# Kernel tuning notes

Measured on AMD Instinct MI355X. Metric: run time of the kernel, lower is better.

The kernel has to match this reference:

```python
import jax, jax.numpy as jnp
import numpy as np

N, L, E, NB, H = 128, 200, 128, 2, 2
ITEM = 50000
TEMP = 0.2
HD = E // H


def _ln(x, g, b, eps=1e-8):
    m = x.mean(-1, keepdims=True)
    v = ((x - m) ** 2).mean(-1, keepdims=True)
    return (x - m) / jnp.sqrt(v + eps) * g + b


def setup_inputs() -> dict:
    key = jax.random.key(0)
    ks = jax.random.split(key, 20)
    rng = np.random.default_rng(0)
    log_seqs = rng.integers(1, ITEM + 1, size=(N, L))
    lens = rng.integers(20, L + 1, size=(N,))
    log_seqs[np.arange(L)[None, :] < (L - lens[:, None])] = 0  # left padding, id 0
    pos_seqs = rng.integers(1, ITEM + 1, size=(N, L))
    neg_seqs = rng.integers(1, ITEM + 1, size=(N, L))
    item_emb = jax.random.normal(ks[0], (ITEM + 1, E), jnp.float32) * 0.02
    item_emb = item_emb.at[0].set(0.0)  # padding_idx=0
    s = 1.0 / np.sqrt(E)
    return {
        "item_emb": item_emb,
        "pos_emb": jax.random.normal(ks[1], (L + 1, E), jnp.float32) * 0.02,
        "W_asp": jax.random.normal(ks[2], (16, E, E), jnp.float32) * s,
        "w_weight": jax.random.normal(ks[3], (2 * E,), jnp.float32) * (1.0 / np.sqrt(2 * E)),
        "w_bias": jnp.zeros((), jnp.float32),
        "attn_ln_g": jnp.ones((NB, E), jnp.float32),
        "attn_ln_b": jnp.zeros((NB, E), jnp.float32),
        "in_proj_w": jax.random.normal(ks[4], (NB, 3 * E, E), jnp.float32) * s,
        "in_proj_b": jnp.zeros((NB, 3 * E), jnp.float32),
        "out_proj_w": jax.random.normal(ks[5], (NB, E, E), jnp.float32) * s,
        "out_proj_b": jnp.zeros((NB, E), jnp.float32),
        "fwd_ln_g": jnp.ones((NB, E), jnp.float32),
        "fwd_ln_b": jnp.zeros((NB, E), jnp.float32),
        "conv1_w": jax.random.normal(ks[6], (NB, E, E), jnp.float32) * s,
        "conv1_b": jnp.zeros((NB, E), jnp.float32),
        "conv2_w": jax.random.normal(ks[7], (NB, E, E), jnp.float32) * s,
        "conv2_b": jnp.zeros((NB, E), jnp.float32),
        "last_ln_g": jnp.ones((E,), jnp.float32),
        "last_ln_b": jnp.zeros((E,), jnp.float32),
        "user_ids": jnp.asarray(rng.integers(0, 100000, size=(N,)), jnp.int32),
        "log_seqs": jnp.asarray(log_seqs, jnp.int32),
        "pos_seqs": jnp.asarray(pos_seqs, jnp.int32),
        "neg_seqs": jnp.asarray(neg_seqs, jnp.int32),
        "epoch": 1,
    }


def reference(item_emb, pos_emb, W_asp, w_weight, w_bias, attn_ln_g, attn_ln_b,
              in_proj_w, in_proj_b, out_proj_w, out_proj_b, fwd_ln_g, fwd_ln_b,
              conv1_w, conv1_b, conv2_w, conv2_b, last_ln_g, last_ln_b,
              user_ids, log_seqs, pos_seqs, neg_seqs, epoch):
    tmask = (log_seqs == 0)                               # (N,L) True=pad
    validL = (~tmask).astype(item_emb.dtype)              # (N,L)
    seqs0 = item_emb[log_seqs] * validL[..., None]
    pos_embs = item_emb[pos_seqs] * validL[..., None]
    neg_embs = item_emb[neg_seqs] * validL[..., None]

    validE = jnp.concatenate([validL, validL[:, -1:]], 1)  # (N,L+1)
    kv_save = jnp.concatenate([seqs0, pos_embs[:, -1:, :]], 1)  # (N,L+1,E)

    def aspects(x, valid, residual):
        a = jnp.einsum('nli,aoi->nlao', x, W_asp)          # 16 expert GEMMs batched
        if residual:
            a = a + x[:, :, None, :]
            a = a / (jnp.linalg.norm(a, axis=-1, keepdims=True) + 1e-8)
        return a * valid[:, :, None, None]

    kv4 = aspects(kv_save, validE, True)                   # (N,L+1,16,E)
    temp = aspects(kv_save, validE, False)
    nvalid = validE.sum()
    cent_loss = jnp.linalg.norm(kv_save * validE[..., None] - temp.mean(2), axis=-1).sum() / nvalid

    norm_x = kv4 / (jnp.linalg.norm(kv4, axis=-1, keepdims=True) + 1e-8)
    pos_s = (norm_x * norm_x).sum(-1)                      # (N,L+1,16)
    ttl = jnp.einsum('nlae,nlbe->nlab', norm_x, norm_x)    # pairwise cosine sims
    mi = -(pos_s / TEMP - jnp.log(jnp.exp(ttl / TEMP).sum(-1)))
    ind_loss = (mi * validE[:, :, None]).sum() / nvalid

    s = kv4.sum(2)                                         # (N,L+1,E)
    q = jnp.cumsum(s, 1) - s                               # exclusive cumsum
    cnt = jnp.cumsum(validE, 1) - validE
    q = q / (16.0 * cnt + 1e-8)[..., None] * validE[..., None]

    w_q, w_a = w_weight[:E], w_weight[E:]

    def gate(qv, a4):                                      # learned softmax gating
        logits = (qv @ w_q)[:, :, None] + a4 @ w_a + w_bias
        w = jax.nn.softmax(logits, axis=2)
        return (a4 * w[..., None]).sum(2)

    re_all = gate(q, kv4)                                  # (N,L+1,E)
    re_emb = re_all[:, :L] + kv4[:, :L].mean(2)

    neg_kv4 = aspects(neg_embs, validL, True)
    q2 = q[:, 1:, :] * validL[..., None]
    neg_t = gate(q2, neg_kv4) + neg_kv4.mean(2)
    pos_t = re_all[:, 1:, :] * validL[..., None] + (kv4[:, 1:] * validL[..., None, None]).mean(2)

    seqs = re_emb * (E ** 0.5) + pos_emb[jnp.arange(L)][None]
    seqs = seqs * validL[..., None]
    causal = jnp.where(jnp.tril(jnp.ones((L, L), bool)), 0.0, -1e9)
    scale = HD ** -0.5
    for i in range(NB):
        Qn = _ln(seqs, attn_ln_g[i], attn_ln_b[i])
        qp = Qn @ in_proj_w[i][:E].T + in_proj_b[i][:E]
        kp = seqs @ in_proj_w[i][E:2 * E].T + in_proj_b[i][E:2 * E]
        vp = seqs @ in_proj_w[i][2 * E:].T + in_proj_b[i][2 * E:]
        sp = lambda x: x.reshape(N, L, H, HD).transpose(0, 2, 1, 3)
        att = jax.nn.softmax(jnp.einsum('nhqd,nhkd->nhqk', sp(qp), sp(kp)) * scale + causal, axis=-1)
        o = jnp.einsum('nhqk,nhkd->nhqd', att, sp(vp)).transpose(0, 2, 1, 3).reshape(N, L, E)
        seqs = Qn + (o @ out_proj_w[i].T + out_proj_b[i])
        seqs = _ln(seqs, fwd_ln_g[i], fwd_ln_b[i])
        h = jax.nn.relu(seqs @ conv1_w[i].T + conv1_b[i])
        seqs = (h @ conv2_w[i].T + conv2_b[i]) + seqs
        seqs = seqs * validL[..., None]
    log_feats = _ln(seqs, last_ln_g, last_ln_b)
    pos_logits = (log_feats * pos_t).sum(-1)
    neg_logits = (log_feats * neg_t).sum(-1)
    return (pos_logits, neg_logits, ind_loss, cent_loss)
```

## Files before the change

### kernel.cpp

```cpp
#include <hip/hip_runtime.h>
#include <hip/hip_bf16.h>
#include <cstddef>

typedef __attribute__((ext_vector_type(8))) short bf16x8;
typedef __attribute__((ext_vector_type(4))) float f32x4;
typedef unsigned short ushort_t;

__device__ __forceinline__ short f2bf(float f) {
    __hip_bfloat16 h = __float2bfloat16(f);
    return __builtin_bit_cast(short, h);
}
__device__ __forceinline__ float bf2f(short s) {
    unsigned u = ((unsigned)(unsigned short)s) << 16;
    return __builtin_bit_cast(float, u);
}
__device__ __forceinline__ unsigned pk2(float a, float b) {
    return (unsigned)(unsigned short)f2bf(a) | ((unsigned)(unsigned short)f2bf(b) << 16);
}

__global__ void cvt_all(const float* __restrict__ s0, const float* __restrict__ s1,
                        const float* __restrict__ s2, const float* __restrict__ s3,
                        const float* __restrict__ s4, ushort_t* __restrict__ dst) {
    const int i = blockIdx.x * 256 + threadIdx.x;
    const int mat = i >> 14;
    const int wm = i & 16383;
    const int blk = wm >> 9;
    const int t = blk >> 2, f = blk & 3;
    const int lane = (wm >> 3) & 63;
    const int j = wm & 7;
    const int g4 = lane >> 4, nn = lane & 15;
    const int srcoff = (t * 16 + nn) * 128 + f * 32 + g4 * 8 + j;
    const float* src; int mbase;
    if (mat < 16)      { src = s0; mbase = mat; }
    else if (mat < 22) { src = s1; mbase = mat - 16; }
    else if (mat < 24) { src = s2; mbase = mat - 22; }
    else if (mat < 26) { src = s3; mbase = mat - 24; }
    else               { src = s4; mbase = mat - 26; }
    dst[i] = (ushort_t)f2bf(src[(size_t)mbase * 16384 + srcoff]);
}

__global__ __launch_bounds__(512, 1) void aspects2_kernel(
        const float* __restrict__ item_emb,
        const int* __restrict__ log_seqs, const int* __restrict__ pos_seqs,
        const int* __restrict__ neg_seqs,
        const ushort_t* __restrict__ Wab,
        const float* __restrict__ w_weight,
        const float* __restrict__ pos_emb,
        float* __restrict__ Gout, float* __restrict__ seqs,
        float* __restrict__ validE, float* __restrict__ validL,
        float* __restrict__ pInd, float* __restrict__ pCent,
        int nLossBlocks) {
    __shared__ ushort_t rsb[32 * 2184];
    __shared__ ushort_t xsb[32 * 136];
    __shared__ ushort_t wal_b[128];
    __shared__ int sidx[32];
    __shared__ float s_red[512];
    __shared__ float s_lg[512];
    __shared__ float s_pos[512];
    __shared__ float vld[32];
    __shared__ float centw[32];
    __shared__ float miw[32];

    const int tid = threadIdx.x;
    const int row0 = blockIdx.x * 32;
    const bool losses = (int)blockIdx.x < nLossBlocks;
    const int lane = tid & 63, w = tid >> 6;
    const int g4 = lane >> 4, nn = lane & 15;

    if (tid < 32) {
        const int rg = row0 + tid;
        int si; float vl;
        if (rg < 25728) {
            const int nq = rg / 201, l = rg % 201;
            if (l < 200) { si = log_seqs[nq * 200 + l]; vl = (si != 0) ? 1.f : 0.f; }
            else { vl = (log_seqs[nq * 200 + 199] != 0) ? 1.f : 0.f; si = pos_seqs[nq * 200 + 199]; }
            validE[rg] = vl;
        } else {
            const int rr = rg - 25728;
            vl = (log_seqs[rr] != 0) ? 1.f : 0.f;
            si = neg_seqs[rr];
            validL[rr] = vl;
        }
        sidx[tid] = si;
        vld[tid] = vl;
    }
    if (tid < 128) wal_b[tid] = (ushort_t)f2bf(w_weight[128 + tid]);
    __syncthreads();

    {
        const int r = tid >> 4, c8 = (tid & 15) * 8;
        const float vl = vld[r];
        const float* px = &item_emb[(size_t)sidx[r] * 128 + c8];
        const float4 a = *(const float4*)px;
        const float4 b = *(const float4*)(px + 4);
        *(int2*)&xsb[r * 136 + c8] = make_int2(
            (int)pk2(a.x * vl, a.y * vl), (int)pk2(a.z * vl, a.w * vl));
        *(int2*)&xsb[r * 136 + c8 + 4] = make_int2(
            (int)pk2(b.x * vl, b.y * vl), (int)pk2(b.z * vl, b.w * vl));
    }
    __syncthreads();

    bf16x8 xf0[4], xf1[4], waf[4];
#pragma unroll
    for (int f = 0; f < 4; ++f) {
        xf0[f] = *(const bf16x8*)&xsb[nn * 136 + f * 32 + g4 * 8];
        xf1[f] = *(const bf16x8*)&xsb[(nn + 16) * 136 + f * 32 + g4 * 8];
        waf[f] = *(const bf16x8*)&wal_b[f * 32 + g4 * 8];
    }

    for (int al = 0; al < 2; ++al) {
        const int a = w * 2 + al;
        const ushort_t* wbase = Wab + (size_t)a * 16384 + lane * 8;
#pragma unroll
        for (int t = 0; t < 8; ++t) {
            f32x4 d0 = {0.f, 0.f, 0.f, 0.f}, d1 = d0;
#pragma unroll
            for (int f = 0; f < 4; ++f) {
                bf16x8 wf = *(const bf16x8*)&wbase[(t * 4 + f) * 512];
                d0 = __builtin_amdgcn_mfma_f32_16x16x32_bf16(wf, xf0[f], d0, 0, 0, 0);
                d1 = __builtin_amdgcn_mfma_f32_16x16x32_bf16(wf, xf1[f], d1, 0, 0, 0);
            }
            const int o0 = t * 16 + g4 * 4;
            const int xs0 = o0 & 4;
            {
                const bf16x8 xb = *(const bf16x8*)&xsb[nn * 136 + (o0 & ~7)];
                *(int2*)&rsb[nn * 2184 + a * 136 + o0] = make_int2(
                    (int)pk2(d0[0] + bf2f(xb[xs0]),     d0[1] + bf2f(xb[xs0 + 1])),
                    (int)pk2(d0[2] + bf2f(xb[xs0 + 2]), d0[3] + bf2f(xb[xs0 + 3])));
            }
            {
                const bf16x8 xb = *(const bf16x8*)&xsb[(nn + 16) * 136 + (o0 & ~7)];
                *(int2*)&rsb[(nn + 16) * 2184 + a * 136 + o0] = make_int2(
                    (int)pk2(d1[0] + bf2f(xb[xs0]),     d1[1] + bf2f(xb[xs0 + 1])),
                    (int)pk2(d1[2] + bf2f(xb[xs0 + 2]), d1[3] + bf2f(xb[xs0 + 3])));
            }
        }
    }
    __syncthreads();

    f32x4 gram0 = {0.f,0.f,0.f,0.f}, gram1 = gram0, gram2 = gram0, gram3 = gram0;
#pragma unroll
    for (int rl = 0; rl < 4; ++rl) {
        const int row = w * 4 + rl;
        f32x4 dgr = {0.f, 0.f, 0.f, 0.f}, dlp = dgr;
#pragma unroll
        for (int f = 0; f < 4; ++f) {
            bf16x8 fr = *(const bf16x8*)&rsb[row * 2184 + nn * 136 + f * 32 + g4 * 8];
            dgr = __builtin_amdgcn_mfma_f32_16x16x32_bf16(fr, fr, dgr, 0, 0, 0);
            dlp = __builtin_amdgcn_mfma_f32_16x16x32_bf16(fr, waf[f], dlp, 0, 0, 0);
        }
        if (rl == 0) gram0 = dgr; else if (rl == 1) gram1 = dgr;
        else if (rl == 2) gram2 = dgr; else gram3 = dgr;
        if (g4 == (nn >> 2)) s_red[row * 16 + nn] = dgr[nn & 3];
        if (nn == 0) {
#pragma unroll
            for (int r = 0; r < 4; ++r) s_lg[row * 16 + g4 * 4 + r] = dlp[r];
        }
    }
    __syncthreads();

    {
        const float nrm = sqrtf(s_red[tid]);
        const float inv1 = 1.f / (nrm + 1e-8f);
        const float n2 = nrm * inv1;
        const float sg = inv1 / (n2 + 1e-8f);
        const float ts = n2 / (n2 + 1e-8f);
        const float logit = s_lg[tid] * inv1;
        float mx = logit;
#pragma unroll
        for (int m = 1; m < 16; m <<= 1) mx = fmaxf(mx, __shfl_xor(mx, m, 16));
        const float e = __expf(logit - mx);
        float ssum = e;
#pragma unroll
        for (int m = 1; m < 16; m <<= 1) ssum += __shfl_xor(ssum, m, 16);
        s_red[tid] = sg;
        s_pos[tid] = ts * ts * 5.f;
        s_lg[tid] = (e / ssum + 0.0625f) * inv1;
    }
    __syncthreads();

    {
        const int row = tid >> 4, ol = tid & 15, o8 = ol * 8;
        float g[8] = {0.f, 0.f, 0.f, 0.f, 0.f, 0.f, 0.f, 0.f};
        float sr[8] = {0.f, 0.f, 0.f, 0.f, 0.f, 0.f, 0.f, 0.f};
#pragma unroll
        for (int a = 0; a < 16; ++a) {
            const bf16x8 vb = *(const bf16x8*)&rsb[row * 2184 + a * 136 + o8];
            const float gw = s_lg[row * 16 + a];
#pragma unroll
            for (int j = 0; j < 8; ++j) {
                const float v = bf2f(vb[j]);
                g[j] += v * gw;
                if (losses) sr[j] += v;
            }
        }
        float* go = &Gout[(size_t)(row0 + row) * 128 + o8];
        *(float4*)go       = make_float4(g[0], g[1], g[2], g[3]);
        *(float4*)(go + 4) = make_float4(g[4], g[5], g[6], g[7]);
        if (losses) {
            const int rg = row0 + row;
            const int nq = rg / 201, l = rg % 201;
            if (l < 200) {
                const float4 p0 = *(const float4*)&pos_emb[l * 128 + o8];
                const float4 p1 = *(const float4*)&pos_emb[l * 128 + o8 + 4];
                const float vv = vld[row];
                float* so = &seqs[(size_t)(nq * 200 + l) * 128 + o8];
                const float SQ = 11.313708498984761f;
                *(float4*)so = make_float4((g[0] * SQ + p0.x) * vv, (g[1] * SQ + p0.y) * vv,
                                           (g[2] * SQ + p0.z) * vv, (g[3] * SQ + p0.w) * vv);
                *(float4*)(so + 4) = make_float4((g[4] * SQ + p1.x) * vv, (g[5] * SQ + p1.y) * vv,
                                                 (g[6] * SQ + p1.z) * vv, (g[7] * SQ + p1.w) * vv);
            }
            const bf16x8 xb = *(const bf16x8*)&xsb[row * 136 + o8];
            float c = 0.f;
#pragma unroll
            for (int j = 0; j < 8; ++j) {
                const float dd = 2.f * bf2f(xb[j]) - sr[j] * 0.0625f;
                c += dd * dd;
            }
            c += __shfl_xor(c, 1, 64);
            c += __shfl_xor(c, 2, 64);
            c += __shfl_xor(c, 4, 64);
            c += __shfl_xor(c, 8, 64);
            if (ol == 0) centw[row] = sqrtf(c) * vld[row];
        }
    }

    if (losses) {
#pragma unroll
        for (int rl = 0; rl < 4; ++rl) {
            const int row = w * 4 + rl;
            const f32x4 dd = (rl == 0) ? gram0 : (rl == 1) ? gram1 : (rl == 2) ? gram2 : gram3;
            const float sgb = s_red[row * 16 + nn];
            float mis = 0.f;
#pragma unroll
            for (int r = 0; r < 4; ++r) {
                const int a = g4 * 4 + r;
                const float sga = s_red[row * 16 + a];
                float eb = __expf(5.f * dd[r] * sga * sgb);
#pragma unroll
                for (int m = 1; m < 16; m <<= 1) eb += __shfl_xor(eb, m, 16);
                mis += -(s_pos[row * 16 + a] - logf(eb));
            }
            mis += __shfl_xor(mis, 16, 64);
            mis += __shfl_xor(mis, 32, 64);
            if (lane == 0) miw[row] = mis * vld[row];
        }
        __syncthreads();
        if (tid == 0) {
            float si = 0.f, sc = 0.f;
#pragma unroll
            for (int r = 0; r < 32; ++r) { si += miw[r]; sc += centw[r]; }
            pInd[blockIdx.x] = si;
            pCent[blockIdx.x] = sc;
        }
    }
}

__global__ __launch_bounds__(256) void qkv_kernel(const float* __restrict__ X,
                                                  const ushort_t* __restrict__ W3,
                                                  const float* __restrict__ b3,
                                                  const float* __restrict__ lng,
                                                  const float* __restrict__ lnb,
                                                  float* __restrict__ Xn,
                                                  ushort_t* __restrict__ qo,
                                                  ushort_t* __restrict__ ko,
                                                  ushort_t* __restrict__ vo) {
    const int tid = threadIdx.x, lane = tid & 63, w = tid >> 6;
    const int q = lane >> 4, nn = lane & 15;
    const int m0 = blockIdx.x * 64 + w * 16;
    float xv[4][8];
    float s = 0.f, sq = 0.f;
    const float* xr = &X[(size_t)(m0 + nn) * 128];
#pragma unroll
    for (int f = 0; f < 4; ++f) {
        const float4 a = *(const float4*)&xr[f * 32 + q * 8];
        const float4 b = *(const float4*)&xr[f * 32 + q * 8 + 4];
        xv[f][0] = a.x; xv[f][1] = a.y; xv[f][2] = a.z; xv[f][3] = a.w;
        xv[f][4] = b.x; xv[f][5] = b.y; xv[f][6] = b.z; xv[f][7] = b.w;
        s += (a.x + a.y) + (a.z + a.w) + (b.x + b.y) + (b.z + b.w);
        sq += (a.x * a.x + a.y * a.y) + (a.z * a.z + a.w * a.w)
            + (b.x * b.x + b.y * b.y) + (b.z * b.z + b.w * b.w);
    }
    bf16x8 afr[4];
#pragma unroll
    for (int f = 0; f < 4; ++f) {
        bf16x8 v;
#pragma unroll
        for (int j = 0; j < 8; ++j) v[j] = f2bf(xv[f][j]);
        afr[f] = v;
    }
    s += __shfl_xor(s, 16, 64);  s += __shfl_xor(s, 32, 64);
    sq += __shfl_xor(sq, 16, 64); sq += __shfl_xor(sq, 32, 64);
    const float mean = s * 0.0078125f;
    const float var = fmaxf(sq * 0.0078125f - mean * mean, 0.f);
    const float inv = rsqrtf(var + 1e-8f);
    bf16x8 afq[4];
#pragma unroll
    for (int f = 0; f < 4; ++f) {
        const int c0 = f * 32 + q * 8;
        const float4 ga = *(const float4*)&lng[c0];
        const float4 gb = *(const float4*)&lng[c0 + 4];
        const float4 ba = *(const float4*)&lnb[c0];
        const float4 bb = *(const float4*)&lnb[c0 + 4];
        float y[8];
        y[0] = (xv[f][0] - mean) * inv * ga.x + ba.x;
        y[1] = (xv[f][1] - mean) * inv * ga.y + ba.y;
        y[2] = (xv[f][2] - mean) * inv * ga.z + ba.z;
        y[3] = (xv[f][3] - mean) * inv * ga.w + ba.w;
        y[4] = (xv[f][4] - mean) * inv * gb.x + bb.x;
        y[5] = (xv[f][5] - mean) * inv * gb.y + bb.y;
        y[6] = (xv[f][6] - mean) * inv * gb.z + bb.z;
        y[7] = (xv[f][7] - mean) * inv * gb.w + bb.w;
        float* xo = &Xn[(size_t)(m0 + nn) * 128 + c0];
        *(float4*)xo       = make_float4(y[0], y[1], y[2], y[3]);
        *(float4*)(xo + 4) = make_float4(y[4], y[5], y[6], y[7]);
        bf16x8 v;
#pragma unroll
        for (int j = 0; j < 8; ++j) v[j] = f2bf(y[j]);
        afq[f] = v;
    }
    ushort_t* const outs[3] = {qo, ko, vo};
#pragma unroll
    for (int mi = 0; mi < 3; ++mi) {
        const ushort_t* wbase = W3 + (size_t)mi * 16384 + lane * 8;
        f32x4 acc[8];
#pragma unroll
        for (int t = 0; t < 8; ++t) acc[t] = (f32x4){0.f, 0.f, 0.f, 0.f};
#pragma unroll
        for (int t = 0; t < 8; ++t) {
#pragma unroll
            for (int f = 0; f < 4; ++f) {
                bf16x8 b = *(const bf16x8*)&wbase[(t * 4 + f) * 512];
                acc[t] = __builtin_amdgcn_mfma_f32_16x16x32_bf16(
                    (mi == 0) ? afq[f] : afr[f], b, acc[t], 0, 0, 0);
            }
        }
        const float* bi = b3 + mi * 128;
        ushort_t* outp = outs[mi];
#pragma unroll
        for (int t = 0; t < 8; ++t) {
            const int n = t * 16 + nn;
            const float bv = bi[n];
#pragma unroll
            for (int r = 0; r < 4; ++r) {
                const int row = m0 + q * 4 + r;
                outp[(size_t)row * 128 + n] = (ushort_t)f2bf(acc[t][r] + bv);
            }
        }
    }
}

__global__ __launch_bounds__(256) void ffn_kernel(const ushort_t* __restrict__ attno,
                                                  const ushort_t* __restrict__ outWb,
                                                  const float* __restrict__ outB,
                                                  const float* __restrict__ resQn,
                                                  const float* __restrict__ lng,
                                                  const float* __restrict__ lnb,
                                                  const ushort_t* __restrict__ c1wb,
                                                  const float* __restrict__ c1b,
                                                  const ushort_t* __restrict__ c2wb,
                                                  const float* __restrict__ c2b,
                                                  const float* __restrict__ validL,
                                                  float* __restrict__ seqs) {
    __shared__ ushort_t hls[64 * 136];
    const int tid = threadIdx.x, lane = tid & 63, w = tid >> 6;
    const int q = lane >> 4, nn = lane & 15;
    const int m0 = blockIdx.x * 64 + w * 16;
    const int wrow = w * 16;

    bf16x8 af[4];
    {
        const ushort_t* xb = &attno[(size_t)(m0 + nn) * 128];
#pragma unroll
        for (int f = 0; f < 4; ++f) af[f] = *(const bf16x8*)&xb[f * 32 + q * 8];
    }
    f32x4 acc[8];
#pragma unroll
    for (int t = 0; t < 8; ++t) acc[t] = (f32x4){0.f, 0.f, 0.f, 0.f};
    {
        const ushort_t* wbase = outWb + lane * 8;
#pragma unroll
        for (int t = 0; t < 8; ++t)
#pragma unroll
            for (int f = 0; f < 4; ++f) {
                bf16x8 b = *(const bf16x8*)&wbase[(t * 4 + f) * 512];
                acc[t] = __builtin_amdgcn_mfma_f32_16x16x32_bf16(af[f], b, acc[t], 0, 0, 0);
            }
    }
    float y[8][4];
    float s[4] = {0.f, 0.f, 0.f, 0.f}, sq[4] = {0.f, 0.f, 0.f, 0.f};
#pragma unroll
    for (int t = 0; t < 8; ++t) {
        const int n = t * 16 + nn;
        const float bi = outB[n];
#pragma unroll
        for (int r = 0; r < 4; ++r) {
            const float v = acc[t][r] + bi + resQn[(size_t)(m0 + q * 4 + r) * 128 + n];
            y[t][r] = v;
            s[r] += v;
            sq[r] += v * v;
        }
    }
#pragma unroll
    for (int m = 1; m < 16; m <<= 1) {
#pragma unroll
        for (int r = 0; r < 4; ++r) {
            s[r] += __shfl_xor(s[r], m, 64);
            sq[r] += __shfl_xor(sq[r], m, 64);
        }
    }
#pragma unroll
    for (int r = 0; r < 4; ++r) {
        const float mean = s[r] * 0.0078125f;
        const float var = fmaxf(sq[r] * 0.0078125f - mean * mean, 0.f);
        const float inv = rsqrtf(var + 1e-8f);
        s[r] = mean; sq[r] = inv;
    }
#pragma unroll
    for (int t = 0; t < 8; ++t) {
        const int n = t * 16 + nn;
        const float g = lng[n], b = lnb[n];
#pragma unroll
        for (int r = 0; r < 4; ++r) {
            const float v = (y[t][r] - s[r]) * sq[r] * g + b;
            y[t][r] = v;
            hls[(wrow + q * 4 + r) * 136 + n] = (ushort_t)f2bf(v);
        }
    }
    __syncthreads();
    {
        const ushort_t* xb = &hls[(wrow + nn) * 136];
#pragma unroll
        for (int f = 0; f < 4; ++f) af[f] = *(const bf16x8*)&xb[f * 32 + q * 8];
    }
    f32x4 acc2[8];
#pragma unroll
    for (int t = 0; t < 8; ++t) acc2[t] = (f32x4){0.f, 0.f, 0.f, 0.f};
    {
        const ushort_t* wbase = c1wb + lane * 8;
#pragma unroll
        for (int t = 0; t < 8; ++t)
#pragma unroll
            for (int f = 0; f < 4; ++f) {
                bf16x8 b = *(const bf16x8*)&wbase[(t * 4 + f) * 512];
                acc2[t] = __builtin_amdgcn_mfma_f32_16x16x32_bf16(af[f], b, acc2[t], 0, 0, 0);
            }
    }
    __syncthreads();
#pragma unroll
    for (int t = 0; t < 8; ++t) {
        const int n = t * 16 + nn;
        const float bi = c1b[n];
#pragma unroll
        for (int r = 0; r < 4; ++r)
            hls[(wrow + q * 4 + r) * 136 + n] = (ushort_t)f2bf(fmaxf(acc2[t][r] + bi, 0.f));
    }
    __syncthreads();
    {
        const ushort_t* xb = &hls[(wrow + nn) * 136];
#pragma unroll
        for (int f = 0; f < 4; ++f) af[f] = *(const bf16x8*)&xb[f * 32 + q * 8];
    }
    f32x4 acc3[8];
#pragma unroll
    for (int t = 0; t < 8; ++t) acc3[t] = (f32x4){0.f, 0.f, 0.f, 0.f};
    {
        const ushort_t* wbase = c2wb + lane * 8;
#pragma unroll
        for (int t = 0; t < 8; ++t)
#pragma unroll
            for (int f = 0; f < 4; ++f) {
                bf16x8 b = *(const bf16x8*)&wbase[(t * 4 + f) * 512];
                acc3[t] = __builtin_amdgcn_mfma_f32_16x16x32_bf16(af[f], b, acc3[t], 0, 0, 0);
            }
    }
    float mk[4];
#pragma unroll
    for (int r = 0; r < 4; ++r) mk[r] = validL[m0 + q * 4 + r];
#pragma unroll
    for (int t = 0; t < 8; ++t) {
        const int n = t * 16 + nn;
        const float bi = c2b[n];
#pragma unroll
        for (int r = 0; r < 4; ++r) {
            const int row = m0 + q * 4 + r;
            seqs[(size_t)row * 128 + n] = (acc3[t][r] + bi + y[t][r]) * mk[r];
        }
    }
}

__global__ void reduce_kernel(const float* __restrict__ pInd, const float* __restrict__ pCent,
                              int nblk, const float* __restrict__ validE, int nve,
                              float* __restrict__ outp) {
    __shared__ float a1[256], a2[256], a3[256];
    const int tid = threadIdx.x;
    float si = 0.f, sc = 0.f, nv = 0.f;
    for (int t = tid; t < nblk; t += 256) { si += pInd[t]; sc += pCent[t]; }
    for (int t = tid; t < nve; t += 256) nv += validE[t];
    a1[tid] = si; a2[tid] = sc; a3[tid] = nv;
    __syncthreads();
    for (int s = 128; s > 0; s >>= 1) {
        if (tid < s) { a1[tid] += a1[tid + s]; a2[tid] += a2[tid + s]; a3[tid] += a3[tid + s]; }
        __syncthreads();
    }
    if (tid == 0) { outp[0] = a1[0] / a3[0]; outp[1] = a2[0] / a3[0]; }
}

__global__ __launch_bounds__(256) void attn_kernel(const ushort_t* __restrict__ qp,
                                                   const ushort_t* __restrict__ kp,
                                                   const ushort_t* __restrict__ vp,
                                                   ushort_t* __restrict__ outp) {
    __shared__ ushort_t KsU[2048];
    __shared__ ushort_t VtU[2560];
    __shared__ ushort_t Pb[2560];

    const int tid = threadIdx.x, lane = tid & 63, w = tid >> 6;
    const int b = blockIdx.x;
    const int nh = b >> 2, qt = b & 3;
    const int n = nh >> 1, h = nh & 1;
    const size_t base = (size_t)n * 200 * 128 + (size_t)h * 64;
    const int qw = qt * 64 + w * 16;
    const bool wactive = qw < 200;
    const int q15 = lane & 15, g4 = lane >> 4;
    const int qglob = qw + q15;

    bf16x8 qf[2];
    {
        const int qr = (qglob < 200) ? qglob : 199;
#pragma unroll
        for (int f = 0; f < 2; ++f)
            qf[f] = *(const bf16x8*)&qp[base + (size_t)qr * 128 + f * 32 + g4 * 8];
    }
    f32x4 Oacc[4];
#pragma unroll
    for (int nt = 0; nt < 4; ++nt) Oacc[nt] = (f32x4){0.f, 0.f, 0.f, 0.f};
    float mrun = -1e30f, lrun = 0.f;

    const int kmax = min(200, qt * 64 + 64);
    ushort_t* PbW = Pb + w * 640;

    for (int jt = 0; jt < kmax; jt += 32) {
        __syncthreads();
        {
            const int k = tid >> 3, e0 = (tid & 7) * 8;
            const int krow = jt + k;
            int4 a = make_int4(0, 0, 0, 0);
            if (krow < 200) a = *(const int4*)&kp[base + (size_t)krow * 128 + e0];
            *(int4*)&KsU[(k * 128 + ((e0 * 2) ^ ((k & 7) << 4))) >> 1] = a;
        }
        {
            const int k = tid & 31, e0 = (tid >> 5) * 8;
            const int vrow = jt + k;
            int4 a = make_int4(0, 0, 0, 0);
            if (vrow < 200) a = *(const int4*)&vp[base + (size_t)vrow * 128 + e0];
            VtU[(e0 + 0) * 40 + k] = (ushort_t)((unsigned)a.x & 0xFFFF);
            VtU[(e0 + 1) * 40 + k] = (ushort_t)((unsigned)a.x >> 16);
            VtU[(e0 + 2) * 40 + k] = (ushort_t)((unsigned)a.y & 0xFFFF);
            VtU[(e0 + 3) * 40 + k] = (ushort_t)((unsigned)a.y >> 16);
            VtU[(e0 + 4) * 40 + k] = (ushort_t)((unsigned)a.z & 0xFFFF);
            VtU[(e0 + 5) * 40 + k] = (ushort_t)((unsigned)a.z >> 16);
            VtU[(e0 + 6) * 40 + k] = (ushort_t)((unsigned)a.w & 0xFFFF);
            VtU[(e0 + 7) * 40 + k] = (ushort_t)((unsigned)a.w >> 16);
        }
        __syncthreads();
        if (!wactive) continue;

        f32x4 d0 = {0.f, 0.f, 0.f, 0.f}, d1 = d0;
#pragma unroll
        for (int f = 0; f < 2; ++f) {
            const int ebyte = g4 * 16 + f * 64;
            const int sw = ebyte ^ ((q15 & 7) << 4);
            bf16x8 a0 = *(const bf16x8*)&KsU[(q15 * 128 + sw) >> 1];
            bf16x8 a1 = *(const bf16x8*)&KsU[((q15 + 16) * 128 + sw) >> 1];
            d0 = __builtin_amdgcn_mfma_f32_16x16x32_bf16(a0, qf[f], d0, 0, 0, 0);
            d1 = __builtin_amdgcn_mfma_f32_16x16x32_bf16(a1, qf[f], d1, 0, 0, 0);
        }
        const int kb = jt + g4 * 4;
        float p[8];
        float tmax = -1e30f;
#pragma unroll
        for (int r = 0; r < 4; ++r) {
            const float s0 = (kb + r      <= qglob) ? d0[r] * 0.125f : -1e30f;
            const float s1 = (kb + r + 16 <= qglob) ? d1[r] * 0.125f : -1e30f;
            p[r] = s0; p[r + 4] = s1;
            tmax = fmaxf(tmax, fmaxf(s0, s1));
        }
        tmax = fmaxf(tmax, __shfl_xor(tmax, 16, 64));
        tmax = fmaxf(tmax, __shfl_xor(tmax, 32, 64));
        const float mnew = fmaxf(mrun, tmax);
        const float corr = __expf(mrun - mnew);
        mrun = mnew;
        float tsum = 0.f;
#pragma unroll
        for (int i = 0; i < 8; ++i) {
            float pe = __expf(p[i] - mnew);
            pe = bf2f(f2bf(pe));
            p[i] = pe;
            tsum += pe;
        }
        tsum += __shfl_xor(tsum, 16, 64);
        tsum += __shfl_xor(tsum, 32, 64);
        lrun = lrun * corr + tsum;
        const int kl = g4 * 4;
        *(unsigned*)&PbW[q15 * 40 + kl]          = pk2(p[0], p[1]);
        *(unsigned*)&PbW[q15 * 40 + kl + 2]      = pk2(p[2], p[3]);
        *(unsigned*)&PbW[q15 * 40 + 16 + kl]     = pk2(p[4], p[5]);
        *(unsigned*)&PbW[q15 * 40 + 16 + kl + 2] = pk2(p[6], p[7]);
        asm volatile("" ::: "memory");
        float corr_r[4];
#pragma unroll
        for (int r = 0; r < 4; ++r) corr_r[r] = __shfl(corr, g4 * 4 + r, 64);
#pragma unroll
        for (int nt = 0; nt < 4; ++nt) {
#pragma unroll
            for (int r = 0; r < 4; ++r) Oacc[nt][r] *= corr_r[r];
        }
        bf16x8 pa = *(const bf16x8*)&PbW[q15 * 40 + g4 * 8];
#pragma unroll
        for (int nt = 0; nt < 4; ++nt) {
            bf16x8 vb = *(const bf16x8*)&VtU[(nt * 16 + q15) * 40 + g4 * 8];
            Oacc[nt] = __builtin_amdgcn_mfma_f32_16x16x32_bf16(pa, vb, Oacc[nt], 0, 0, 0);
        }
    }
    if (wactive) {
        float linv[4];
#pragma unroll
        for (int r = 0; r < 4; ++r) linv[r] = 1.f / __shfl(lrun, g4 * 4 + r, 64);
#pragma unroll
        for (int r = 0; r < 4; ++r) {
            const int qg = qw + g4 * 4 + r;
            if (qg < 200) {
#pragma unroll
                for (int nt = 0; nt < 4; ++nt)
                    outp[base + (size_t)qg * 128 + nt * 16 + q15] =
                        (ushort_t)f2bf(Oacc[nt][r] * linv[r]);
            }
        }
    }
}

__global__ __launch_bounds__(256) void logits_kernel(const float* __restrict__ seqs,
                                                     const float* __restrict__ lastg,
                                                     const float* __restrict__ lastb,
                                                     const float* __restrict__ G,
                                                     const float* __restrict__ negt,
                                                     const float* __restrict__ validL,
                                                     float* __restrict__ outp) {
    const int row = blockIdx.x * 4 + (threadIdx.x >> 6);
    const int lane = threadIdx.x & 63;
    if (row >= 25600) return;
    const int n = row / 200, j = row % 200;
    const float2 x = *(const float2*)&seqs[(size_t)row * 128 + lane * 2];
    float s = x.x + x.y, sq = x.x * x.x + x.y * x.y;
#pragma unroll
    for (int m = 1; m < 64; m <<= 1) { s += __shfl_xor(s, m, 64); sq += __shfl_xor(sq, m, 64); }
    const float mean = s * 0.0078125f;
    const float var = fmaxf(sq * 0.0078125f - mean * mean, 0.f);
    const float inv = rsqrtf(var + 1e-8f);
    const float2 gg = *(const float2*)&lastg[lane * 2];
    const float2 bb = *(const float2*)&lastb[lane * 2];
    const float y0 = (x.x - mean) * inv * gg.x + bb.x;
    const float y1 = (x.y - mean) * inv * gg.y + bb.y;
    const float2 g2 = *(const float2*)&G[((size_t)n * 201 + j + 1) * 128 + lane * 2];
    const float2 t2 = *(const float2*)&negt[(size_t)row * 128 + lane * 2];
    float sp = y0 * g2.x + y1 * g2.y;
    float sn = y0 * t2.x + y1 * t2.y;
#pragma unroll
    for (int m = 1; m < 64; m <<= 1) { sp += __shfl_xor(sp, m, 64); sn += __shfl_xor(sn, m, 64); }
    if (lane == 0) { outp[row] = sp * validL[row]; outp[25600 + row] = sn; }
}

extern "C" void kernel_launch(void* const* d_in, const int* in_sizes, int n_in,
                              void* d_out, int out_size, void* d_ws, size_t ws_size,
                              hipStream_t stream) {
    (void)in_sizes; (void)n_in; (void)out_size; (void)ws_size;
    const float* item_emb = (const float*)d_in[0];
    const float* pos_emb  = (const float*)d_in[1];
    const float* W_asp    = (const float*)d_in[2];
    const float* w_weight = (const float*)d_in[3];
    const float* attn_g = (const float*)d_in[5];
    const float* attn_b = (const float*)d_in[6];
    const float* inW    = (const float*)d_in[7];
    const float* inB    = (const float*)d_in[8];
    const float* outW   = (const float*)d_in[9];
    const float* outB   = (const float*)d_in[10];
    const float* fwd_g  = (const float*)d_in[11];
    const float* fwd_b  = (const float*)d_in[12];
    const float* c1w    = (const float*)d_in[13];
    const float* c1b    = (const float*)d_in[14];
    const float* c2w    = (const float*)d_in[15];
    const float* c2b    = (const float*)d_in[16];
    const float* last_g = (const float*)d_in[17];
    const float* last_b = (const float*)d_in[18];
    const int* log_seqs = (const int*)d_in[20];
    const int* pos_seqs = (const int*)d_in[21];
    const int* neg_seqs = (const int*)d_in[22];

    float* ws = (float*)d_ws;
    const size_t S = (size_t)128 * 201 * 128;
    ushort_t* qp = (ushort_t*)ws;
    ushort_t* kp = qp + (size_t)25600 * 128;
    float* G     = ws + 2 * S;
    float* negt  = ws + 3 * S;
    float* seqs  = ws + 4 * S;
    float* Qn    = ws + 5 * S;
    ushort_t* vp    = (ushort_t*)(ws + 6 * S);
    ushort_t* attno = (ushort_t*)(ws + 7 * S);
    ushort_t* wb  = (ushort_t*)(ws + 8 * S);
    ushort_t* Wab  = wb;
    ushort_t* inWb = Wab + 262144;
    ushort_t* outWb = inWb + 98304;
    ushort_t* c1b_w = outWb + 32768;
    ushort_t* c2b_w = c1b_w + 32768;
    float* validE = ws + 8 * S + 229376;
    float* validL = validE + 128 * 201;
    float* pInd   = validL + 128 * 200;
    float* pCent  = pInd + 804;
    float* outF   = (float*)d_out;

    cvt_all<<<dim3(1792), dim3(256), 0, stream>>>(W_asp, inW, outW, c1w, c2w, wb);
    aspects2_kernel<<<dim3(1604), dim3(512), 0, stream>>>(
        item_emb, log_seqs, pos_seqs, neg_seqs, Wab, w_weight, pos_emb,
        G, seqs, validE, validL, pInd, pCent, 804);
    reduce_kernel<<<dim3(1), dim3(256), 0, stream>>>(
        pInd, pCent, 804, validE, 128 * 201, outF + 51200);

    for (int i = 0; i < 2; ++i) {
        qkv_kernel<<<dim3(400), dim3(256), 0, stream>>>(
            seqs, inWb + (size_t)i * 3 * 16384, inB + (size_t)i * 384,
            attn_g + i * 128, attn_b + i * 128, Qn, qp, kp, vp);
        attn_kernel<<<dim3(1024), dim3(256), 0, stream>>>(qp, kp, vp, attno);
        ffn_kernel<<<dim3(400), dim3(256), 0, stream>>>(
            attno, outWb + (size_t)i * 16384, outB + i * 128, Qn,
            fwd_g + i * 128, fwd_b + i * 128,
            c1b_w + (size_t)i * 16384, c1b + i * 128,
            c2b_w + (size_t)i * 16384, c2b + i * 128,
            validL, seqs);
    }
    logits_kernel<<<dim3(6400), dim3(256), 0, stream>>>(
        seqs, last_g, last_b, G, negt, validL, outF);
}
```

Baseline: 218.5 us.

## Fuse final layernorm and logits into last FFN, fold residual into aspect weights

The final layer norm and pos/neg logit dot products now run inside the last FFN kernel's epilogue, using 16-lane shuffles over the MFMA accumulators. This removes the separate logits kernel and the write and re-read of seqs for the last block. Separately, the aspect-projection residual (x + W x) is folded into the bf16 weight conversion by adding an identity to W_asp, so the per-element add from shared memory disappears from the aspects kernel. The fused epilogue reads G and negt with scattered per-lane loads, and adding 1.0 to the diagonal before bf16 rounding slightly changes numerics.

```diff
diff --git a/kernel.cpp b/kernel.cpp
--- a/kernel.cpp
+++ b/kernel.cpp
@@ -29,14 +29,18 @@
     const int lane = (wm >> 3) & 63;
     const int j = wm & 7;
     const int g4 = lane >> 4, nn = lane & 15;
-    const int srcoff = (t * 16 + nn) * 128 + f * 32 + g4 * 8 + j;
+    const int o = t * 16 + nn;
+    const int k = f * 32 + g4 * 8 + j;
+    const int srcoff = o * 128 + k;
     const float* src; int mbase;
     if (mat < 16)      { src = s0; mbase = mat; }
     else if (mat < 22) { src = s1; mbase = mat - 16; }
     else if (mat < 24) { src = s2; mbase = mat - 22; }
     else if (mat < 26) { src = s3; mbase = mat - 24; }
     else               { src = s4; mbase = mat - 26; }
-    dst[i] = (ushort_t)f2bf(src[(size_t)mbase * 16384 + srcoff]);
+    float v = src[(size_t)mbase * 16384 + srcoff];
+    if (mat < 16 && o == k) v += 1.f;
+    dst[i] = (ushort_t)f2bf(v);
 }
 
 __global__ __launch_bounds__(512, 1) void aspects2_kernel(
@@ -121,19 +125,10 @@
                 d1 = __builtin_amdgcn_mfma_f32_16x16x32_bf16(wf, xf1[f], d1, 0, 0, 0);
             }
             const int o0 = t * 16 + g4 * 4;
-            const int xs0 = o0 & 4;
-            {
-                const bf16x8 xb = *(const bf16x8*)&xsb[nn * 136 + (o0 & ~7)];
-                *(int2*)&rsb[nn * 2184 + a * 136 + o0] = make_int2(
-                    (int)pk2(d0[0] + bf2f(xb[xs0]),     d0[1] + bf2f(xb[xs0 + 1])),
-                    (int)pk2(d0[2] + bf2f(xb[xs0 + 2]), d0[3] + bf2f(xb[xs0 + 3])));
-            }
-            {
-                const bf16x8 xb = *(const bf16x8*)&xsb[(nn + 16) * 136 + (o0 & ~7)];
-                *(int2*)&rsb[(nn + 16) * 2184 + a * 136 + o0] = make_int2(
-                    (int)pk2(d1[0] + bf2f(xb[xs0]),     d1[1] + bf2f(xb[xs0 + 1])),
-                    (int)pk2(d1[2] + bf2f(xb[xs0 + 2]), d1[3] + bf2f(xb[xs0 + 3])));
-            }
+            *(int2*)&rsb[nn * 2184 + a * 136 + o0] = make_int2(
+                (int)pk2(d0[0], d0[1]), (int)pk2(d0[2], d0[3]));
+            *(int2*)&rsb[(nn + 16) * 2184 + a * 136 + o0] = make_int2(
+                (int)pk2(d1[0], d1[1]), (int)pk2(d1[2], d1[3]));
         }
     }
     __syncthreads();
@@ -351,6 +346,7 @@
     }
 }
 
+template <int LAST>
 __global__ __launch_bounds__(256) void ffn_kernel(const ushort_t* __restrict__ attno,
                                                   const ushort_t* __restrict__ outWb,
                                                   const float* __restrict__ outB,
@@ -362,7 +358,12 @@
                                                   const ushort_t* __restrict__ c2wb,
                                                   const float* __restrict__ c2b,
                                                   const float* __restrict__ validL,
-                                                  float* __restrict__ seqs) {
+                                                  float* __restrict__ seqs,
+                                                  const float* __restrict__ lastg,
+                                                  const float* __restrict__ lastb,
+                                                  const float* __restrict__ G,
+                                                  const float* __restrict__ negt,
+                                                  float* __restrict__ outp) {
     __shared__ ushort_t hls[64 * 136];
     const int tid = threadIdx.x, lane = tid & 63, w = tid >> 6;
     const int q = lane >> 4, nn = lane & 15;
@@ -478,14 +479,83 @@
     float mk[4];
 #pragma unroll
     for (int r = 0; r < 4; ++r) mk[r] = validL[m0 + q * 4 + r];
-#pragma unroll
-    for (int t = 0; t < 8; ++t) {
-        const int n = t * 16 + nn;
-        const float bi = c2b[n];
+
+    if constexpr (!LAST) {
+#pragma unroll
+        for (int t = 0; t < 8; ++t) {
+            const int n = t * 16 + nn;
+            const float bi = c2b[n];
+#pragma unroll
+            for (int r = 0; r < 4; ++r) {
+                const int row = m0 + q * 4 + r;
+                seqs[(size_t)row * 128 + n] = (acc3[t][r] + bi + y[t][r]) * mk[r];
+            }
+        }
+    } else {
+        float ov[8][4];
+        float s2[4] = {0.f, 0.f, 0.f, 0.f}, q2[4] = {0.f, 0.f, 0.f, 0.f};
+#pragma unroll
+        for (int t = 0; t < 8; ++t) {
+            const int n = t * 16 + nn;
+            const float bi = c2b[n];
+#pragma unroll
+            for (int r = 0; r < 4; ++r) {
+                const float v = (acc3[t][r] + bi + y[t][r]) * mk[r];
+                ov[t][r] = v;
+                s2[r] += v;
+                q2[r] += v * v;
+            }
+        }
+#pragma unroll
+        for (int m = 1; m < 16; m <<= 1) {
+#pragma unroll
+            for (int r = 0; r < 4; ++r) {
+                s2[r] += __shfl_xor(s2[r], m, 64);
+                q2[r] += __shfl_xor(q2[r], m, 64);
+            }
+        }
+#pragma unroll
+        for (int r = 0; r < 4; ++r) {
+            const float mean = s2[r] * 0.0078125f;
+            const float var = fmaxf(q2[r] * 0.0078125f - mean * mean, 0.f);
+            const float inv = rsqrtf(var + 1e-8f);
+            s2[r] = mean; q2[r] = inv;
+        }
+        float sp[4] = {0.f, 0.f, 0.f, 0.f}, sn[4] = {0.f, 0.f, 0.f, 0.f};
+        int nqr[4], lr[4];
 #pragma unroll
         for (int r = 0; r < 4; ++r) {
             const int row = m0 + q * 4 + r;
-            seqs[(size_t)row * 128 + n] = (acc3[t][r] + bi + y[t][r]) * mk[r];
+            nqr[r] = row / 200;
+            lr[r] = row - nqr[r] * 200;
+        }
+#pragma unroll
+        for (int t = 0; t < 8; ++t) {
+            const int n = t * 16 + nn;
+            const float g = lastg[n], b = lastb[n];
+#pragma unroll
+            for (int r = 0; r < 4; ++r) {
+                const int row = m0 + q * 4 + r;
+                const float yln = (ov[t][r] - s2[r]) * q2[r] * g + b;
+                sp[r] += yln * G[((size_t)nqr[r] * 201 + lr[r] + 1) * 128 + n];
+                sn[r] += yln * negt[(size_t)row * 128 + n];
+            }
+        }
+#pragma unroll
+        for (int m = 1; m < 16; m <<= 1) {
+#pragma unroll
+            for (int r = 0; r < 4; ++r) {
+                sp[r] += __shfl_xor(sp[r], m, 64);
+                sn[r] += __shfl_xor(sn[r], m, 64);
+            }
+        }
+        if (nn == 0) {
+#pragma unroll
+            for (int r = 0; r < 4; ++r) {
+                const int row = m0 + q * 4 + r;
+                outp[row] = sp[r] * mk[r];
+                outp[25600 + row] = sn[r];
+            }
         }
     }
 }
@@ -638,37 +708,6 @@
             }
         }
     }
-}
-
-__global__ __launch_bounds__(256) void logits_kernel(const float* __restrict__ seqs,
-                                                     const float* __restrict__ lastg,
-                                                     const float* __restrict__ lastb,
-                                                     const float* __restrict__ G,
-                                                     const float* __restrict__ negt,
-                                                     const float* __restrict__ validL,
-                                                     float* __restrict__ outp) {
-    const int row = blockIdx.x * 4 + (threadIdx.x >> 6);
-    const int lane = threadIdx.x & 63;
-    if (row >= 25600) return;
-    const int n = row / 200, j = row % 200;
-    const float2 x = *(const float2*)&seqs[(size_t)row * 128 + lane * 2];
-    float s = x.x + x.y, sq = x.x * x.x + x.y * x.y;
-#pragma unroll
-    for (int m = 1; m < 64; m <<= 1) { s += __shfl_xor(s, m, 64); sq += __shfl_xor(sq, m, 64); }
-    const float mean = s * 0.0078125f;
-    const float var = fmaxf(sq * 0.0078125f - mean * mean, 0.f);
-    const float inv = rsqrtf(var + 1e-8f);
-    const float2 gg = *(const float2*)&lastg[lane * 2];
-    const float2 bb = *(const float2*)&lastb[lane * 2];
-    const float y0 = (x.x - mean) * inv * gg.x + bb.x;
-    const float y1 = (x.y - mean) * inv * gg.y + bb.y;
-    const float2 g2 = *(const float2*)&G[((size_t)n * 201 + j + 1) * 128 + lane * 2];
-    const float2 t2 = *(const float2*)&negt[(size_t)row * 128 + lane * 2];
-    float sp = y0 * g2.x + y1 * g2.y;
-    float sn = y0 * t2.x + y1 * t2.y;
-#pragma unroll
-    for (int m = 1; m < 64; m <<= 1) { sp += __shfl_xor(sp, m, 64); sn += __shfl_xor(sn, m, 64); }
-    if (lane == 0) { outp[row] = sp * validL[row]; outp[25600 + row] = sn; }
 }
 
 extern "C" void kernel_launch(void* const* d_in, const int* in_sizes, int n_in,
@@ -731,13 +770,20 @@
             seqs, inWb + (size_t)i * 3 * 16384, inB + (size_t)i * 384,
             attn_g + i * 128, attn_b + i * 128, Qn, qp, kp, vp);
         attn_kernel<<<dim3(1024), dim3(256), 0, stream>>>(qp, kp, vp, attno);
-        ffn_kernel<<<dim3(400), dim3(256), 0, stream>>>(
-            attno, outWb + (size_t)i * 16384, outB + i * 128, Qn,
-            fwd_g + i * 128, fwd_b + i * 128,
-            c1b_w + (size_t)i * 16384, c1b + i * 128,
-            c2b_w + (size_t)i * 16384, c2b + i * 128,
-            validL, seqs);
-    }
-    logits_kernel<<<dim3(6400), dim3(256), 0, stream>>>(
-        seqs, last_g, last_b, G, negt, validL, outF);
-}
+        if (i == 0) {
+            ffn_kernel<0><<<dim3(400), dim3(256), 0, stream>>>(
+                attno, outWb + (size_t)i * 16384, outB + i * 128, Qn,
+                fwd_g + i * 128, fwd_b + i * 128,
+                c1b_w + (size_t)i * 16384, c1b + i * 128,
+                c2b_w + (size_t)i * 16384, c2b + i * 128,
+                validL, seqs, nullptr, nullptr, nullptr, nullptr, nullptr);
+        } else {
+            ffn_kernel<1><<<dim3(400), dim3(256), 0, stream>>>(
+                attno, outWb + (size_t)i * 16384, outB + i * 128, Qn,
+                fwd_g + i * 128, fwd_b + i * 128,
+                c1b_w + (size_t)i * 16384, c1b + i * 128,
+                c2b_w + (size_t)i * 16384, c2b + i * 128,
+                validL, nullptr, last_g, last_b, G, negt, outF);
+        }
+    }
+}
```

Result: faster. 206.7 us (-5.4%).
